# Performance work log

Hardware: AMD Instinct MI355X
Metric: run time of the kernel (lower is better)

The kernel has to match this reference:

```python
import jax, jax.numpy as jnp
import numpy as np

B, C, H, W = 16, 256, 96, 96
PLANES = 64            # inplanes * ratio = 256 * 0.25
HEADS = 4
EPS = 1e-5             # BatchNorm eps


def setup_inputs() -> dict:
    key = jax.random.key(0)
    ks = jax.random.split(key, 8)
    HW = H * W
    G = HW // HEADS    # group size of the grouped 1x1 conv over spatial-positions-as-channels
    return {
        "x": jax.random.normal(ks[0], (B, C, H, W), jnp.float32),
        # input_conv: Conv1x1(C->PLANES) -> BN -> ReLU -> Conv1x1(PLANES->C)
        "w1": jax.random.normal(ks[1], (PLANES, C), jnp.float32) * (1.0 / np.sqrt(C)),
        "b1": jax.random.normal(ks[2], (PLANES,), jnp.float32) * 0.01,
        "gamma": jnp.ones((PLANES,), jnp.float32),
        "beta": jnp.zeros((PLANES,), jnp.float32),
        "mean": jnp.zeros((PLANES,), jnp.float32),
        "var": jnp.ones((PLANES,), jnp.float32),
        "w2": jax.random.normal(ks[3], (C, PLANES), jnp.float32) * (1.0 / np.sqrt(PLANES)),
        "b2": jax.random.normal(ks[4], (C,), jnp.float32) * 0.01,
        # conv_mask: Conv2d(HW, HEADS, k=1, groups=HEADS) -> weight [HEADS, G], bias [HEADS]
        "wm": jax.random.normal(ks[5], (HEADS, G), jnp.float32) * (1.0 / np.sqrt(G)),
        "bm": jax.random.normal(ks[6], (HEADS,), jnp.float32) * 0.01,
    }


def reference(x, w1, b1, gamma, beta, mean, var, w2, b2, wm, bm):
    Bx, Cx, Hx, Wx = x.shape
    G = (Hx * Wx) // HEADS
    # ---- input_conv: 1x1 conv -> BN (inference) -> ReLU -> 1x1 conv ----
    h = jnp.einsum('bchw,pc->bphw', x, w1) + b1[None, :, None, None]
    scale = (gamma / jnp.sqrt(var + EPS))[None, :, None, None]
    h = jax.nn.relu((h - mean[None, :, None, None]) * scale + beta[None, :, None, None])
    y = jnp.einsum('bphw,cp->bchw', h, w2) + b2[None, :, None, None]
    # ---- treat spatial positions as channels: [B, HEADS, G, C] ----
    ix = y.transpose(0, 2, 3, 1).reshape(Bx, HEADS, G, Cx)
    # grouped 1x1 conv over HW-channels -> logits [B, HEADS, C]
    logits = jnp.einsum('bhgc,hg->bhc', ix, wm) + bm[None, :, None]
    # softmax over channel axis (torch dim=2 of [B, HEADS, C, 1])
    mask = jax.nn.softmax(logits, axis=2)
    # context pooling matmul: [B,HEADS,G,C] @ [B,HEADS,C,1] -> [B,HEADS,G]
    ctx = jnp.einsum('bhgc,bhc->bhg', ix, mask)
    context = ctx.reshape(Bx, 1, Hx, Wx)
    # fusion_types = ('channel_add',)
    return x + context
```

## Files before the change

kernel.cpp:

```cpp
#include <hip/hip_runtime.h>

#define Bn 16
#define Cn 256
#define HWn 9216
#define Pn 64
#define HEADSn 4
#define Gn 2304
#define STILE 64
#define TILES_PER_B (HWn / STILE)
#define NBLK (Bn * TILES_PER_B)

typedef float f32x4 __attribute__((ext_vector_type(4)));
typedef short short4v __attribute__((ext_vector_type(4)));
typedef short short8 __attribute__((ext_vector_type(8)));

static __device__ __forceinline__ unsigned short f2bf(float f) {
    unsigned int b = __builtin_bit_cast(unsigned int, f);
    unsigned int r = b + 0x7FFFu + ((b >> 16) & 1u);
    return (unsigned short)(r >> 16);
}
static __device__ __forceinline__ float bf2f(unsigned short u) {
    unsigned int b = ((unsigned int)u) << 16;
    return __builtin_bit_cast(float, b);
}
static __device__ __forceinline__ void gload_lds16(const void* g, void* l) {
    __builtin_amdgcn_global_load_lds((const __attribute__((address_space(1))) void*)g,
                                     (__attribute__((address_space(3))) void*)l, 16, 0, 0);
}

__global__ __launch_bounds__(256)
void k0_prep(const float* __restrict__ w1, const float* __restrict__ b1,
             const float* __restrict__ gamma, const float* __restrict__ beta,
             const float* __restrict__ mean, const float* __restrict__ var,
             float* __restrict__ scbc, short* __restrict__ w1s)
{
    const int gid = blockIdx.x * 256 + threadIdx.x;
    if (gid < 2048) {
        const int row = gid >> 5;
        const int kc  = (gid & 31) << 3;
        const float* p = w1 + row * Cn + kc;
        short8 v;
        #pragma unroll
        for (int j = 0; j < 8; ++j) v[j] = (short)f2bf(p[j]);
        const int idx = (row * Cn + kc) ^ ((row & 7) << 3);
        *reinterpret_cast<short8*>(&w1s[idx]) = v;
    }
    if (gid < Pn) {
        float s = gamma[gid] * rsqrtf(var[gid] + 1e-5f);
        scbc[gid] = s;
        scbc[Pn + gid] = (b1[gid] - mean[gid]) * s + beta[gid];
    }
}

__global__ __launch_bounds__(256)
void k1_gemm(const float* __restrict__ x, const short* __restrict__ w1s,
             const float* __restrict__ scbc, const float* __restrict__ wm,
             float* __restrict__ hmp, short* __restrict__ hg)
{
    __shared__ short w1l[Pn * Cn];
    __shared__ short xl[Cn * STILE];
    __shared__ float hml[Pn];

    const int bid  = blockIdx.x;
    const int b    = bid / TILES_PER_B;
    const int tile = bid % TILES_PER_B;
    const int s0   = tile * STILE;
    const int t    = threadIdx.x;
    const int lane = t & 63;
    const int wv   = t >> 6;
    const int g    = lane >> 4;
    const int m16  = lane & 15;
    const int sbase = wv * 16 + m16;

    #pragma unroll
    for (int i = 0; i < 8; ++i) {
        const int chunk = i * 4 + wv;
        gload_lds16(w1s + chunk * 512 + lane * 8, &w1l[chunk * 512]);
    }

    const int c0 = t >> 4;
    const int s4 = t & 15;
    const float* xb = x + (size_t)b * Cn * HWn + s0 + s4 * 4;
    f32x4 xa[16];
    #pragma unroll
    for (int i = 0; i < 16; ++i)
        xa[i] = *reinterpret_cast<const f32x4*>(xb + (size_t)(c0 + 16 * i) * HWn);

    if (t < Pn) hml[t] = 0.f;

    #pragma unroll
    for (int i = 0; i < 16; ++i) {
        const int c = c0 + 16 * i;
        short4v v;
        #pragma unroll
        for (int j = 0; j < 4; ++j) v[j] = (short)f2bf(xa[i][j]);
        const int f   = (c & 7) ^ ((c >> 3) & 3);
        const int idx = (c * STILE + s4 * 4) ^ (f << 3);
        *reinterpret_cast<short4v*>(&xl[idx]) = v;
    }
    __syncthreads();

    f32x4 acc[4] = { {0,0,0,0}, {0,0,0,0}, {0,0,0,0}, {0,0,0,0} };
    #pragma unroll
    for (int ks = 0; ks < 8; ++ks) {
        short8 bf;
        #pragma unroll
        for (int j = 0; j < 8; ++j) {
            const int k = ks * 32 + g * 8 + j;
            bf[j] = xl[(k * STILE + sbase) ^ ((j ^ g) << 3)];
        }
        #pragma unroll
        for (int rt = 0; rt < 4; ++rt) {
            const int row = rt * 16 + m16;
            const int idx = (row * Cn + ks * 32 + g * 8) ^ ((row & 7) << 3);
            const short8 af = *reinterpret_cast<const short8*>(&w1l[idx]);
            acc[rt] = __builtin_amdgcn_mfma_f32_16x16x32_bf16(af, bf, acc[rt], 0, 0, 0);
        }
    }

    float h[4][4];
    #pragma unroll
    for (int rt = 0; rt < 4; ++rt) {
        #pragma unroll
        for (int r = 0; r < 4; ++r) {
            const int p = rt * 16 + g * 4 + r;
            const float hv = acc[rt][r] * scbc[p] + scbc[Pn + p];
            h[rt][r] = hv > 0.f ? hv : 0.f;
        }
    }

    const float wmv = wm[s0 + sbase];
    #pragma unroll
    for (int rt = 0; rt < 4; ++rt) {
        #pragma unroll
        for (int r = 0; r < 4; ++r) {
            float v = h[rt][r] * wmv;
            v += __shfl_xor(v, 1); v += __shfl_xor(v, 2);
            v += __shfl_xor(v, 4); v += __shfl_xor(v, 8);
            if (m16 == 0) atomicAdd(&hml[rt * 16 + g * 4 + r], v);
        }
    }
    __syncthreads();

    short* ht = xl;
    #pragma unroll
    for (int rt = 0; rt < 4; ++rt) {
        short4v hv;
        #pragma unroll
        for (int r = 0; r < 4; ++r) hv[r] = (short)f2bf(h[rt][r]);
        *reinterpret_cast<short4v*>(&ht[sbase * 72 + rt * 16 + g * 4]) = hv;
    }
    __syncthreads();

    {
        const int s = t >> 2, q = t & 3;
        const short8 a0 = *reinterpret_cast<const short8*>(&ht[s * 72 + q * 16]);
        const short8 a1 = *reinterpret_cast<const short8*>(&ht[s * 72 + q * 16 + 8]);
        short* dst = hg + ((size_t)b * HWn + s0 + s) * Pn + q * 16;
        *reinterpret_cast<short8*>(dst)     = a0;
        *reinterpret_cast<short8*>(dst + 8) = a1;
    }
    if (t < Pn) hmp[bid * Pn + t] = hml[t];
}

__global__ __launch_bounds__(256)
void k2_mask(const float* __restrict__ hmp, const float* __restrict__ w2,
             const float* __restrict__ b2, const float* __restrict__ wm,
             float* __restrict__ wmix, float* __restrict__ bmix)
{
    __shared__ float hms[Pn];
    __shared__ float masks[Cn];
    __shared__ float red[4];
    __shared__ float part[4][Pn];

    const int bh = blockIdx.x;
    const int head = bh & (HEADSn - 1);
    const int t = threadIdx.x;
    const int l = t & 63;
    const int wv = t >> 6;

    {
        const int p = t & 63, q = t >> 6;
        const float* base = hmp + ((size_t)(bh >> 2) * TILES_PER_B + (bh & 3) * 36) * Pn;
        float sp = 0.f;
        #pragma unroll
        for (int j = 0; j < 9; ++j) sp += base[(q + 4 * j) * Pn + p];
        part[q][p] = sp;
    }
    __syncthreads();
    if (t < Pn) hms[t] = part[0][t] + part[1][t] + part[2][t] + part[3][t];
    __syncthreads();

    float wsum = 0.f;
    for (int i = t; i < Gn; i += 256) wsum += wm[head * Gn + i];
    #pragma unroll
    for (int d = 1; d < 64; d <<= 1) wsum += __shfl_xor(wsum, d);
    if (l == 0) red[wv] = wsum;
    __syncthreads();
    wsum = red[0] + red[1] + red[2] + red[3];

    float lg = 0.f;
    #pragma unroll
    for (int k = 0; k < Pn; ++k) lg = fmaf(w2[t * Pn + k], hms[k], lg);
    lg = fmaf(b2[t], wsum, lg);

    float mx = lg;
    #pragma unroll
    for (int d = 1; d < 64; d <<= 1) mx = fmaxf(mx, __shfl_xor(mx, d));
    __syncthreads();
    if (l == 0) red[wv] = mx;
    __syncthreads();
    mx = fmaxf(fmaxf(red[0], red[1]), fmaxf(red[2], red[3]));
    const float ev = __expf(lg - mx);
    float sm = ev;
    #pragma unroll
    for (int d = 1; d < 64; d <<= 1) sm += __shfl_xor(sm, d);
    __syncthreads();
    if (l == 0) red[wv] = sm;
    __syncthreads();
    sm = red[0] + red[1] + red[2] + red[3];
    masks[t] = ev / sm;
    __syncthreads();

    {
        const int k = t & (Pn - 1);
        const int q = t >> 6;
        float wp = 0.f;
        #pragma unroll
        for (int i = 0; i < 64; ++i) {
            const int c = q * 64 + i;
            wp = fmaf(masks[c], w2[c * Pn + k], wp);
        }
        part[q][k] = wp;
    }
    __syncthreads();
    if (t < Pn) wmix[bh * Pn + t] = part[0][t] + part[1][t] + part[2][t] + part[3][t];

    float bp = masks[t] * b2[t];
    #pragma unroll
    for (int d = 1; d < 64; d <<= 1) bp += __shfl_xor(bp, d);
    __syncthreads();
    if (l == 0) red[wv] = bp;
    __syncthreads();
    if (t == 0) bmix[bh] = red[0] + red[1] + red[2] + red[3];
}

__global__ __launch_bounds__(256)
void k3_stream(const float* __restrict__ x, const short* __restrict__ hg,
               const float* __restrict__ wmix, const float* __restrict__ bmix,
               float* __restrict__ out)
{
    __shared__ float ctxl[STILE];

    const int bid  = blockIdx.x;
    const int b    = bid / TILES_PER_B;
    const int tile = bid % TILES_PER_B;
    const int s0   = tile * STILE;
    const int head = s0 / Gn;
    const int bh   = b * HEADSn + head;
    const int t    = threadIdx.x;

    if (t < STILE) {
        const short* hr = hg + ((size_t)b * HWn + s0 + t) * Pn;
        const float* wmx = wmix + bh * Pn;
        float acc = 0.f;
        #pragma unroll
        for (int i = 0; i < 8; ++i) {
            const short8 v = *reinterpret_cast<const short8*>(hr + i * 8);
            const f32x4 w0 = *reinterpret_cast<const f32x4*>(wmx + i * 8);
            const f32x4 w1v = *reinterpret_cast<const f32x4*>(wmx + i * 8 + 4);
            #pragma unroll
            for (int j = 0; j < 4; ++j) {
                acc = fmaf(bf2f((unsigned short)v[j]), w0[j], acc);
                acc = fmaf(bf2f((unsigned short)v[4 + j]), w1v[j], acc);
            }
        }
        ctxl[t] = acc + bmix[bh];
    }
    __syncthreads();

    const int c0 = t >> 4;
    const int s4 = t & 15;
    const f32x4 cv = *reinterpret_cast<const f32x4*>(&ctxl[s4 * 4]);
    const float* xb = x + (size_t)b * Cn * HWn + s0 + s4 * 4;
    float* ob = out + (size_t)b * Cn * HWn + s0 + s4 * 4;
    #pragma unroll
    for (int i = 0; i < 16; ++i) {
        const size_t off = (size_t)(c0 + 16 * i) * HWn;
        *reinterpret_cast<f32x4*>(ob + off) =
            *reinterpret_cast<const f32x4*>(xb + off) + cv;
    }
}

extern "C" void kernel_launch(void* const* d_in, const int* in_sizes, int n_in,
                              void* d_out, int out_size, void* d_ws, size_t ws_size,
                              hipStream_t stream)
{
    (void)in_sizes; (void)n_in; (void)out_size; (void)ws_size;
    const float* x     = (const float*)d_in[0];
    const float* w1    = (const float*)d_in[1];
    const float* b1    = (const float*)d_in[2];
    const float* gamma = (const float*)d_in[3];
    const float* beta  = (const float*)d_in[4];
    const float* mean  = (const float*)d_in[5];
    const float* var   = (const float*)d_in[6];
    const float* w2    = (const float*)d_in[7];
    const float* b2    = (const float*)d_in[8];
    const float* wm    = (const float*)d_in[9];

    float* out  = (float*)d_out;
    float* wsf  = (float*)d_ws;
    float* hmp  = wsf;
    float* wmix = hmp + NBLK * Pn;
    float* bmix = wmix + Bn * HEADSn * Pn;
    float* scbc = bmix + 64;
    short* w1s  = (short*)(scbc + 128);
    short* hg   = w1s + Pn * Cn;

    k0_prep<<<dim3(8), dim3(256), 0, stream>>>(w1, b1, gamma, beta, mean, var, scbc, w1s);
    k1_gemm<<<dim3(NBLK), dim3(256), 0, stream>>>(x, w1s, scbc, wm, hmp, hg);
    k2_mask<<<dim3(Bn * HEADSn), dim3(256), 0, stream>>>(hmp, w2, b2, wm, wmix, bmix);
    k3_stream<<<dim3(NBLK), dim3(256), 0, stream>>>(x, hg, wmix, bmix, out);
}
```

Before: 107.9 us.

## Make k1 persistent over nine tiles with double-buffered x prefetch

The GEMM kernel now has each block process nine consecutive 64-position tiles instead of one. It loads W1 into LDS once per block and prefetches the next x tile into registers while the current tile runs through MFMA, using a double-buffered LDS tile. The h output is stored straight from registers instead of being staged through LDS. The head-mask partial sums are accumulated in registers across tiles, which shrinks the hmp partials that k2 must reduce. In exchange the grid drops to 256 blocks, about one per CU, so the change risks lower occupancy and weaker latency hiding, plus less coalesced direct stores of h.

```diff
diff --git a/kernel.cpp b/kernel.cpp
--- a/kernel.cpp
+++ b/kernel.cpp
@@ -8,7 +8,9 @@
 #define Gn 2304
 #define STILE 64
 #define TILES_PER_B (HWn / STILE)
-#define NBLK (Bn * TILES_PER_B)
+#define NTILE (Bn * TILES_PER_B)
+#define CHUNK 9
+#define NBLK (NTILE / CHUNK)
 
 typedef float f32x4 __attribute__((ext_vector_type(4)));
 typedef short short4v __attribute__((ext_vector_type(4)));
@@ -58,13 +60,12 @@
              float* __restrict__ hmp, short* __restrict__ hg)
 {
     __shared__ short w1l[Pn * Cn];
-    __shared__ short xl[Cn * STILE];
-    __shared__ float hml[Pn];
-
-    const int bid  = blockIdx.x;
-    const int b    = bid / TILES_PER_B;
-    const int tile = bid % TILES_PER_B;
-    const int s0   = tile * STILE;
+    __shared__ short xl[2][Cn * STILE];
+    __shared__ float hml[4][Pn];
+
+    const int pid  = blockIdx.x;
+    const int b    = pid / 16;
+    const int t0b  = pid * CHUNK - b * TILES_PER_B;
     const int t    = threadIdx.x;
     const int lane = t & 63;
     const int wv   = t >> 6;
@@ -80,87 +81,125 @@
 
     const int c0 = t >> 4;
     const int s4 = t & 15;
-    const float* xb = x + (size_t)b * Cn * HWn + s0 + s4 * 4;
-    f32x4 xa[16];
-    #pragma unroll
-    for (int i = 0; i < 16; ++i)
-        xa[i] = *reinterpret_cast<const f32x4*>(xb + (size_t)(c0 + 16 * i) * HWn);
-
-    if (t < Pn) hml[t] = 0.f;
-
-    #pragma unroll
-    for (int i = 0; i < 16; ++i) {
-        const int c = c0 + 16 * i;
-        short4v v;
-        #pragma unroll
-        for (int j = 0; j < 4; ++j) v[j] = (short)f2bf(xa[i][j]);
-        const int f   = (c & 7) ^ ((c >> 3) & 3);
-        const int idx = (c * STILE + s4 * 4) ^ (f << 3);
-        *reinterpret_cast<short4v*>(&xl[idx]) = v;
-    }
-    __syncthreads();
-
-    f32x4 acc[4] = { {0,0,0,0}, {0,0,0,0}, {0,0,0,0}, {0,0,0,0} };
-    #pragma unroll
-    for (int ks = 0; ks < 8; ++ks) {
-        short8 bf;
-        #pragma unroll
-        for (int j = 0; j < 8; ++j) {
-            const int k = ks * 32 + g * 8 + j;
-            bf[j] = xl[(k * STILE + sbase) ^ ((j ^ g) << 3)];
-        }
-        #pragma unroll
-        for (int rt = 0; rt < 4; ++rt) {
-            const int row = rt * 16 + m16;
-            const int idx = (row * Cn + ks * 32 + g * 8) ^ ((row & 7) << 3);
-            const short8 af = *reinterpret_cast<const short8*>(&w1l[idx]);
-            acc[rt] = __builtin_amdgcn_mfma_f32_16x16x32_bf16(af, bf, acc[rt], 0, 0, 0);
-        }
-    }
-
-    float h[4][4];
-    #pragma unroll
-    for (int rt = 0; rt < 4; ++rt) {
+    const float* xbb = x + (size_t)b * Cn * HWn + s4 * 4;
+    short* hgb = hg + (size_t)b * HWn * Pn;
+    const float* scp = scbc;
+
+    float sc[4][4], bc[4][4];
+    #pragma unroll
+    for (int rt = 0; rt < 4; ++rt)
         #pragma unroll
         for (int r = 0; r < 4; ++r) {
             const int p = rt * 16 + g * 4 + r;
-            const float hv = acc[rt][r] * scbc[p] + scbc[Pn + p];
-            h[rt][r] = hv > 0.f ? hv : 0.f;
-        }
-    }
-
-    const float wmv = wm[s0 + sbase];
-    #pragma unroll
-    for (int rt = 0; rt < 4; ++rt) {
+            sc[rt][r] = scp[p];
+            bc[rt][r] = scp[Pn + p];
+        }
+
+    float hmacc[4][4];
+    #pragma unroll
+    for (int rt = 0; rt < 4; ++rt)
+        #pragma unroll
+        for (int r = 0; r < 4; ++r) hmacc[rt][r] = 0.f;
+
+    {
+        const float* xb = xbb + (size_t)(t0b * STILE);
+        f32x4 xa[16];
+        #pragma unroll
+        for (int i = 0; i < 16; ++i)
+            xa[i] = *reinterpret_cast<const f32x4*>(xb + (size_t)(c0 + 16 * i) * HWn);
+        #pragma unroll
+        for (int i = 0; i < 16; ++i) {
+            const int c = c0 + 16 * i;
+            short4v v;
+            #pragma unroll
+            for (int j = 0; j < 4; ++j) v[j] = (short)f2bf(xa[i][j]);
+            const int f   = (c & 7) ^ ((c >> 3) & 3);
+            const int idx = (c * STILE + s4 * 4) ^ (f << 3);
+            *reinterpret_cast<short4v*>(&xl[0][idx]) = v;
+        }
+    }
+    __syncthreads();
+
+    int cur = 0;
+    for (int it = 0; it < CHUNK; ++it) {
+        const int s0 = (t0b + it) * STILE;
+
+        f32x4 xn[16];
+        if (it < CHUNK - 1) {
+            const float* xb = xbb + (size_t)(s0 + STILE);
+            #pragma unroll
+            for (int i = 0; i < 16; ++i)
+                xn[i] = *reinterpret_cast<const f32x4*>(xb + (size_t)(c0 + 16 * i) * HWn);
+        }
+
+        const short* xc = xl[cur];
+        f32x4 acc[4] = { {0,0,0,0}, {0,0,0,0}, {0,0,0,0}, {0,0,0,0} };
+        #pragma unroll
+        for (int ks = 0; ks < 8; ++ks) {
+            short8 bf;
+            #pragma unroll
+            for (int j = 0; j < 8; ++j) {
+                const int k = ks * 32 + g * 8 + j;
+                bf[j] = xc[(k * STILE + sbase) ^ ((j ^ g) << 3)];
+            }
+            #pragma unroll
+            for (int rt = 0; rt < 4; ++rt) {
+                const int row = rt * 16 + m16;
+                const int idx = (row * Cn + ks * 32 + g * 8) ^ ((row & 7) << 3);
+                const short8 af = *reinterpret_cast<const short8*>(&w1l[idx]);
+                acc[rt] = __builtin_amdgcn_mfma_f32_16x16x32_bf16(af, bf, acc[rt], 0, 0, 0);
+            }
+        }
+
+        const float wmv = wm[s0 + sbase];
+        short* hrow = hgb + (size_t)(s0 + sbase) * Pn;
+        #pragma unroll
+        for (int rt = 0; rt < 4; ++rt) {
+            short4v hv;
+            #pragma unroll
+            for (int r = 0; r < 4; ++r) {
+                float h = acc[rt][r] * sc[rt][r] + bc[rt][r];
+                h = h > 0.f ? h : 0.f;
+                hmacc[rt][r] = fmaf(h, wmv, hmacc[rt][r]);
+                hv[r] = (short)f2bf(h);
+            }
+            *reinterpret_cast<short4v*>(hrow + rt * 16 + g * 4) = hv;
+        }
+
+        if (it < CHUNK - 1) {
+            #pragma unroll
+            for (int i = 0; i < 16; ++i) {
+                const int c = c0 + 16 * i;
+                short4v v;
+                #pragma unroll
+                for (int j = 0; j < 4; ++j) v[j] = (short)f2bf(xn[i][j]);
+                const int f   = (c & 7) ^ ((c >> 3) & 3);
+                const int idx = (c * STILE + s4 * 4) ^ (f << 3);
+                *reinterpret_cast<short4v*>(&xl[cur ^ 1][idx]) = v;
+            }
+            __syncthreads();
+            cur ^= 1;
+        }
+    }
+
+    #pragma unroll
+    for (int rt = 0; rt < 4; ++rt)
         #pragma unroll
         for (int r = 0; r < 4; ++r) {
-            float v = h[rt][r] * wmv;
+            float v = hmacc[rt][r];
             v += __shfl_xor(v, 1); v += __shfl_xor(v, 2);
             v += __shfl_xor(v, 4); v += __shfl_xor(v, 8);
-            if (m16 == 0) atomicAdd(&hml[rt * 16 + g * 4 + r], v);
-        }
-    }
-    __syncthreads();
-
-    short* ht = xl;
-    #pragma unroll
-    for (int rt = 0; rt < 4; ++rt) {
-        short4v hv;
-        #pragma unroll
-        for (int r = 0; r < 4; ++r) hv[r] = (short)f2bf(h[rt][r]);
-        *reinterpret_cast<short4v*>(&ht[sbase * 72 + rt * 16 + g * 4]) = hv;
-    }
-    __syncthreads();
-
-    {
-        const int s = t >> 2, q = t & 3;
-        const short8 a0 = *reinterpret_cast<const short8*>(&ht[s * 72 + q * 16]);
-        const short8 a1 = *reinterpret_cast<const short8*>(&ht[s * 72 + q * 16 + 8]);
-        short* dst = hg + ((size_t)b * HWn + s0 + s) * Pn + q * 16;
-        *reinterpret_cast<short8*>(dst)     = a0;
-        *reinterpret_cast<short8*>(dst + 8) = a1;
-    }
-    if (t < Pn) hmp[bid * Pn + t] = hml[t];
+            hmacc[rt][r] = v;
+        }
+    if (m16 == 0) {
+        #pragma unroll
+        for (int rt = 0; rt < 4; ++rt) {
+            f32x4 hv = { hmacc[rt][0], hmacc[rt][1], hmacc[rt][2], hmacc[rt][3] };
+            *reinterpret_cast<f32x4*>(&hml[wv][rt * 16 + g * 4]) = hv;
+        }
+    }
+    __syncthreads();
+    if (t < Pn) hmp[pid * Pn + t] = hml[0][t] + hml[1][t] + hml[2][t] + hml[3][t];
 }
 
 __global__ __launch_bounds__(256)
@@ -181,11 +220,7 @@
 
     {
         const int p = t & 63, q = t >> 6;
-        const float* base = hmp + ((size_t)(bh >> 2) * TILES_PER_B + (bh & 3) * 36) * Pn;
-        float sp = 0.f;
-        #pragma unroll
-        for (int j = 0; j < 9; ++j) sp += base[(q + 4 * j) * Pn + p];
-        part[q][p] = sp;
+        part[q][p] = hmp[(bh * 4 + q) * Pn + p];
     }
     __syncthreads();
     if (t < Pn) hms[t] = part[0][t] + part[1][t] + part[2][t] + part[3][t];
@@ -320,5 +355,5 @@
     k0_prep<<<dim3(8), dim3(256), 0, stream>>>(w1, b1, gamma, beta, mean, var, scbc, w1s);
     k1_gemm<<<dim3(NBLK), dim3(256), 0, stream>>>(x, w1s, scbc, wm, hmp, hg);
     k2_mask<<<dim3(Bn * HEADSn), dim3(256), 0, stream>>>(hmp, w2, b2, wm, wmix, bmix);
-    k3_stream<<<dim3(NBLK), dim3(256), 0, stream>>>(x, hg, wmix, bmix, out);
-}
+    k3_stream<<<dim3(NTILE / 1), dim3(256), 0, stream>>>(x, hg, wmix, bmix, out);
+}
```

After: 101.6 us. 5.9% less time.
